# Kernel optimization log

Hardware: AMD Instinct MI355X
Metric: run time of the kernel (lower is better)

The kernel has to match this reference:

```python
import jax, jax.numpy as jnp
import numpy as np

EMB = 1024
NH = 16
HD = EMB // NH
FF = 4 * EMB
B, T = 2, 2048
LN_EPS = 1e-5


def setup_inputs() -> dict:
    key = jax.random.key(0)
    ks = jax.random.split(key, 16)
    s = 0.02
    return {
        "x": jax.random.normal(ks[0], (B, T, EMB), jnp.float32),
        "wq": jax.random.normal(ks[1], (EMB, EMB), jnp.float32) * s,
        "bq": jnp.zeros((EMB,), jnp.float32),
        "wk": jax.random.normal(ks[2], (EMB, EMB), jnp.float32) * s,
        "bk": jnp.zeros((EMB,), jnp.float32),
        "wv": jax.random.normal(ks[3], (EMB, EMB), jnp.float32) * s,
        "bv": jnp.zeros((EMB,), jnp.float32),
        "wo": jax.random.normal(ks[4], (EMB, EMB), jnp.float32) * s,
        "bo": jnp.zeros((EMB,), jnp.float32),
        "w1": jax.random.normal(ks[5], (EMB, FF), jnp.float32) * s,
        "b1": jnp.zeros((FF,), jnp.float32),
        "w2": jax.random.normal(ks[6], (FF, EMB), jnp.float32) * s,
        "b2": jnp.zeros((EMB,), jnp.float32),
        "ln1_g": jnp.ones((EMB,), jnp.float32),
        "ln1_b": jnp.zeros((EMB,), jnp.float32),
        "ln2_g": jnp.ones((EMB,), jnp.float32),
        "ln2_b": jnp.zeros((EMB,), jnp.float32),
        "alpha_attn": jnp.float32(0.5),
        "alpha_ff": jnp.float32(0.5),
    }


def _layernorm(x, g, b):
    mu = jnp.mean(x, axis=-1, keepdims=True)
    var = jnp.var(x, axis=-1, keepdims=True)
    return (x - mu) * jax.lax.rsqrt(var + LN_EPS) * g + b


def reference(x, wq, bq, wk, bk, wv, bv, wo, bo, w1, b1, w2, b2,
              ln1_g, ln1_b, ln2_g, ln2_b, alpha_attn, alpha_ff):
    residual = x
    x_ = _layernorm(x, ln1_g, ln1_b)
    # [B,T,E] -> [B,H,T,D]
    def heads(y):
        return y.reshape(B, T, NH, HD).transpose(0, 2, 1, 3)
    q = heads(x_ @ wq + bq)
    k = heads(x_ @ wk + bk)
    v = heads(x_ @ wv + bv)
    scores = jnp.einsum("bhqd,bhkd->bhqk", q, k) / np.sqrt(HD).astype(np.float32)
    causal = jnp.tril(jnp.ones((T, T), dtype=bool))
    scores = jnp.where(causal, scores, -jnp.inf)
    attn = jax.nn.softmax(scores, axis=-1)  # dropout is identity in eval mode
    out = jnp.einsum("bhqk,bhkd->bhqd", attn, v)
    out = out.transpose(0, 2, 1, 3).reshape(B, T, EMB)
    out = out @ wo + bo
    x = residual + alpha_attn * out
    x2 = _layernorm(x, ln2_g, ln2_b)
    ff = jax.nn.gelu(x2 @ w1 + b1, approximate=False) @ w2 + b2
    return x + alpha_ff * ff
```

## Files before the change

### kernel.cpp

```cpp
#include <hip/hip_runtime.h>
#include <cmath>

#define EMB 1024
#define NH 16
#define HD 64
#define FF_DIM 4096
#define BB 2
#define TT 2048
#define NTOK (BB * TT)
#define QKVS 3072
#define SC2F 0.18033688011112042f

typedef _Float16 f16x8 __attribute__((ext_vector_type(8)));
typedef _Float16 f16x4 __attribute__((ext_vector_type(4)));
typedef float f32x4 __attribute__((ext_vector_type(4)));

__device__ __forceinline__ float gelu_fast(float x) {
    float u = x * (1.f + 0.044715f * x * x);
    float e = exp2f(u * 2.302118751f);
    return x - x / (e + 1.f);
}

template <typename TIN>
__global__ __launch_bounds__(256) void ln_kernel(const TIN* __restrict__ xin,
                                                 _Float16* __restrict__ out,
                                                 const float* __restrict__ g,
                                                 const float* __restrict__ bv) {
    int tid = threadIdx.x;
    size_t base = (size_t)blockIdx.x * EMB;
    float v[4];
#pragma unroll
    for (int i = 0; i < 4; ++i) v[i] = (float)xin[base + i * 256 + tid];
    float s = v[0] + v[1] + v[2] + v[3];
    float ss = v[0] * v[0] + v[1] * v[1] + v[2] * v[2] + v[3] * v[3];
#pragma unroll
    for (int off = 32; off > 0; off >>= 1) {
        s += __shfl_down(s, off);
        ss += __shfl_down(ss, off);
    }
    __shared__ float red[8];
    int wave = tid >> 6;
    if ((tid & 63) == 0) { red[wave] = s; red[4 + wave] = ss; }
    __syncthreads();
    s = red[0] + red[1] + red[2] + red[3];
    ss = red[4] + red[5] + red[6] + red[7];
    float mu = s * (1.0f / EMB);
    float var = ss * (1.0f / EMB) - mu * mu;
    float rstd = rsqrtf(var + 1e-5f);
#pragma unroll
    for (int i = 0; i < 4; ++i) {
        int idx = i * 256 + tid;
        float y = (v[i] - mu) * rstd * g[idx] + bv[idx];
        out[base + idx] = (_Float16)y;
    }
}

__global__ __launch_bounds__(256) void prep0_kernel(const float* __restrict__ x,
                                                    _Float16* __restrict__ xn,
                                                    const float* __restrict__ ln1_g,
                                                    const float* __restrict__ ln1_b,
                                                    const float* __restrict__ wq,
                                                    const float* __restrict__ wk,
                                                    const float* __restrict__ wv,
                                                    const float* __restrict__ wo,
                                                    const float* __restrict__ bq,
                                                    const float* __restrict__ bk,
                                                    const float* __restrict__ bv,
                                                    _Float16* __restrict__ wqkvT,
                                                    _Float16* __restrict__ woT,
                                                    float* __restrict__ qkvbias) {
    __shared__ float tile[32][33];
    int blk = blockIdx.x;
    int tid = threadIdx.x;
    if (blk >= 4108) {
        size_t base = (size_t)(blk - 4108) * EMB;
        float v[4];
#pragma unroll
        for (int i = 0; i < 4; ++i) v[i] = x[base + i * 256 + tid];
        float s = v[0] + v[1] + v[2] + v[3];
        float ss = v[0] * v[0] + v[1] * v[1] + v[2] * v[2] + v[3] * v[3];
#pragma unroll
        for (int off = 32; off > 0; off >>= 1) {
            s += __shfl_down(s, off);
            ss += __shfl_down(ss, off);
        }
        float* red = &tile[0][0];
        int wave = tid >> 6;
        if ((tid & 63) == 0) { red[wave] = s; red[4 + wave] = ss; }
        __syncthreads();
        s = red[0] + red[1] + red[2] + red[3];
        ss = red[4] + red[5] + red[6] + red[7];
        float mu = s * (1.0f / EMB);
        float var = ss * (1.0f / EMB) - mu * mu;
        float rstd = rsqrtf(var + 1e-5f);
#pragma unroll
        for (int i = 0; i < 4; ++i) {
            int idx = i * 256 + tid;
            xn[base + idx] = (_Float16)((v[i] - mu) * rstd * ln1_g[idx] + ln1_b[idx]);
        }
        return;
    }
    if (blk >= 4096) {
        int i = (blk - 4096) * 256 + tid;
        qkvbias[i] = i < 1024 ? bq[i] : (i < 2048 ? bk[i - 1024] : bv[i - 2048]);
        return;
    }
    const float* W;
    _Float16* Wt;
    int t = blk & 1023;
    int z = blk >> 10;
    if (z == 0) { W = wq; Wt = wqkvT; }
    else if (z == 1) { W = wk; Wt = wqkvT + 1024 * 1024; }
    else if (z == 2) { W = wv; Wt = wqkvT + 2 * 1024 * 1024; }
    else { W = wo; Wt = woT; }
    int bx = (t & 31) * 32, by = (t >> 5) * 32;
    int tx = tid & 31, ty = tid >> 5;
#pragma unroll
    for (int i = 0; i < 32; i += 8)
        tile[ty + i][tx] = W[(size_t)(by + ty + i) * EMB + bx + tx];
    __syncthreads();
#pragma unroll
    for (int i = 0; i < 32; i += 8)
        Wt[(size_t)(bx + ty + i) * EMB + by + tx] = (_Float16)tile[tx][ty + i];
}

__global__ __launch_bounds__(256) void prep2_kernel(const float* __restrict__ w1,
                                                    const float* __restrict__ w2,
                                                    _Float16* __restrict__ w1T,
                                                    _Float16* __restrict__ w2T) {
    int b = blockIdx.x;
    const float* W;
    _Float16* Wt;
    int K, N, t;
    if (b < 4096) { W = w1; Wt = w1T; K = 1024; N = 4096; t = b; }
    else { W = w2; Wt = w2T; K = 4096; N = 1024; t = b - 4096; }
    int ntx = N >> 5;
    int bx = (t % ntx) * 32, by = (t / ntx) * 32;
    __shared__ float tile[32][33];
    int tx = threadIdx.x & 31, ty = threadIdx.x >> 5;
#pragma unroll
    for (int i = 0; i < 32; i += 8)
        tile[ty + i][tx] = W[(size_t)(by + ty + i) * N + bx + tx];
    __syncthreads();
#pragma unroll
    for (int i = 0; i < 32; i += 8)
        Wt[(size_t)(bx + ty + i) * K + by + tx] = (_Float16)tile[tx][ty + i];
}

__global__ __launch_bounds__(256) void vT_kernel(const _Float16* __restrict__ qkv,
                                                 _Float16* __restrict__ VtG) {
    __shared__ _Float16 tile[64][72];
    int tid = threadIdx.x;
    int bh = blockIdx.y;
    int b = bh >> 4, h = bh & 15;
    int t0 = blockIdx.x * 64;
    const _Float16* src = qkv + (size_t)b * TT * QKVS + 2048 + h * HD;
    int r = tid >> 3;
    int c8 = (tid & 7) * 8;
#pragma unroll
    for (int p = 0; p < 2; ++p)
        *(f16x8*)(&tile[r + p * 32][c8]) =
            *(const f16x8*)(src + (size_t)(t0 + r + p * 32) * QKVS + c8);
    __syncthreads();
#pragma unroll
    for (int p = 0; p < 2; ++p) {
        int d = r + p * 32;
        f16x8 v;
#pragma unroll
        for (int j = 0; j < 8; ++j) v[j] = tile[c8 + j][d];
        *(f16x8*)(VtG + ((size_t)bh * HD + d) * TT + t0 + c8) = v;
    }
}

template <int MODE>
__global__ __launch_bounds__(256) void gemm_f16t(const _Float16* __restrict__ A,
                                                 const _Float16* __restrict__ Bt,
                                                 const float* __restrict__ bias,
                                                 void* __restrict__ outp,
                                                 void* __restrict__ vtg,
                                                 int M, int N, int K, int lda, int ldb) {
    __shared__ _Float16 As[128][64];
    __shared__ _Float16 Bs[128][64];
    int tid = threadIdx.x;
    int lane = tid & 63, w = tid >> 6;
    int quad = lane >> 4, l15 = lane & 15;
    int wm = (w >> 1) * 64, wn = (w & 1) * 64;
    int bM = blockIdx.y * 128, bN = blockIdx.x * 128;
    int lr = lane >> 3;
    int lcs = ((lane & 7) ^ lr) * 8;
    int sw = l15 & 7;
    f32x4 acc[4][4] = {};

    const _Float16* Abase = A + (size_t)(bM + w * 32 + lr) * lda + lcs;
    const _Float16* Bbase = Bt + (size_t)(bN + w * 32 + lr) * ldb + lcs;

    for (int kt = 0; kt < K; kt += 64) {
#pragma unroll
        for (int i = 0; i < 4; ++i) {
            __builtin_amdgcn_global_load_lds(
                (const __attribute__((address_space(1))) void*)(Abase + (size_t)(i * 8) * lda + kt),
                (__attribute__((address_space(3))) void*)(&As[w * 32 + i * 8][0]), 16, 0, 0);
            __builtin_amdgcn_global_load_lds(
                (const __attribute__((address_space(1))) void*)(Bbase + (size_t)(i * 8) * ldb + kt),
                (__attribute__((address_space(3))) void*)(&Bs[w * 32 + i * 8][0]), 16, 0, 0);
        }
        __syncthreads();
#pragma unroll
        for (int ks = 0; ks < 2; ++ks) {
            f16x8 af[4], bf[4];
#pragma unroll
            for (int i = 0; i < 4; ++i) {
                int sc = ((ks * 4 + quad) ^ sw) * 8;
                af[i] = *(const f16x8*)(&As[wm + i * 16 + l15][sc]);
                bf[i] = *(const f16x8*)(&Bs[wn + i * 16 + l15][sc]);
            }
#pragma unroll
            for (int i = 0; i < 4; ++i)
#pragma unroll
                for (int j = 0; j < 4; ++j)
                    acc[i][j] = __builtin_amdgcn_mfma_f32_16x16x32_f16(af[i], bf[j], acc[i][j], 0, 0, 0);
        }
        __syncthreads();
    }

    if (MODE == 6 && vtg != nullptr && bN >= 2048) {
        int bb = bM >> 11;
        int tbase = (bM & 2047) + wm;
#pragma unroll
        for (int i = 0; i < 4; ++i)
#pragma unroll
            for (int j = 0; j < 4; ++j) {
                int hd = bN - 2048 + wn + j * 16;
                int col = 2048 + hd + l15;
                _Float16* dst = (_Float16*)vtg +
                    (((size_t)(bb * 16 + (hd >> 6)) * 64) + (hd & 63) + l15) * TT +
                    tbase + i * 16 + quad * 4;
                f16x4 ov;
#pragma unroll
                for (int r = 0; r < 4; ++r) ov[r] = (_Float16)(acc[i][j][r] + bias[col]);
                *(f16x4*)dst = ov;
            }
        return;
    }

#pragma unroll
    for (int i = 0; i < 4; ++i)
#pragma unroll
        for (int j = 0; j < 4; ++j)
#pragma unroll
            for (int r = 0; r < 4; ++r) {
                int row = bM + wm + i * 16 + quad * 4 + r;
                int col = bN + wn + j * 16 + l15;
                size_t idx = (size_t)row * N + col;
                float vv = acc[i][j][r] + bias[col];
                if (MODE == 6) {
                    if (bN < 1024) vv *= SC2F;
                    ((_Float16*)outp)[idx] = (_Float16)vv;
                } else {
                    ((_Float16*)outp)[idx] = (_Float16)gelu_fast(vv);
                }
            }
}

#define STAGE_PAIR(OB, TN, I)                                                            \
    {                                                                                    \
        size_t ko = (size_t)(TN) * 64;                                                   \
        __builtin_amdgcn_global_load_lds(                                                \
            (const __attribute__((address_space(1))) void*)(Ab + (size_t)((I) * 8) * lda + ko), \
            (__attribute__((address_space(3))) void*)(&As[OB][w * 32 + (I) * 8][0]), 16, 0, 0); \
        __builtin_amdgcn_global_load_lds(                                                \
            (const __attribute__((address_space(1))) void*)(Bb + (size_t)((I) * 8) * ldb + ko), \
            (__attribute__((address_space(3))) void*)(&Bs[OB][w * 32 + (I) * 8][0]), 16, 0, 0); \
    }
#define RD_A(CB, I, KS) (*(const f16x8*)(&As[CB][wr * 128 + (I) * 16 + l15][(((KS)*4 + quad) ^ sw) * 8]))
#define RD_B(CB, J, KS) (*(const f16x8*)(&Bs[CB][wc * 64 + (J) * 16 + l15][(((KS)*4 + quad) ^ sw) * 8]))
#define MMQ(I0, J0)                                                                      \
    _Pragma("unroll") for (int ks = 0; ks < 2; ++ks) {                                   \
        _Pragma("unroll") for (int ii = 0; ii < 4; ++ii) {                               \
            _Pragma("unroll") for (int jj = 0; jj < 2; ++jj)                             \
                acc[(I0) + ii][(J0) + jj] = __builtin_amdgcn_mfma_f32_16x16x32_f16(      \
                    af[ii][ks], bf[(J0) + jj][ks], acc[(I0) + ii][(J0) + jj], 0, 0, 0);  \
        }                                                                                \
    }

template <int MODE>
__global__ __launch_bounds__(512, 2) void gemm256(const _Float16* __restrict__ A,
                                                  const _Float16* __restrict__ Bt,
                                                  const float* __restrict__ bias,
                                                  void* __restrict__ outp,
                                                  void* __restrict__ vtg,
                                                  int M, int N, int K, int lda, int ldb) {
    __shared__ _Float16 As[2][256][64];
    __shared__ _Float16 Bs[2][256][64];
    int tid = threadIdx.x;
    int lane = tid & 63, w = tid >> 6;
    int quad = lane >> 4, l15 = lane & 15;
    int wr = w >> 2, wc = w & 3;
    int gx = gridDim.x;
    int nwg = gx * gridDim.y;
    int bid = blockIdx.y * gx + blockIdx.x;
    int cpx = nwg >> 3;
    int sbid = (bid & 7) * cpx + (bid >> 3);
    int bN = (sbid % gx) * 256;
    int bM = (sbid / gx) * 256;
    int lr = lane >> 3;
    int lcs = ((lane & 7) ^ lr) * 8;
    int sw = l15 & 7;
    f32x4 acc[8][4] = {};
    f16x8 af[4][2], bf[4][2];

    const _Float16* Ab = A + (size_t)(bM + w * 32 + lr) * lda + lcs;
    const _Float16* Bb = Bt + (size_t)(bN + w * 32 + lr) * ldb + lcs;
    const int NT = K >> 6;

#pragma unroll
    for (int i = 0; i < 4; ++i) STAGE_PAIR(0, 0, i);
    asm volatile("s_waitcnt vmcnt(0)" ::: "memory");
    __builtin_amdgcn_s_barrier();

    int cur = 0;
    for (int t = 0; t < NT; ++t) {
        int nxt = cur ^ 1;
        int tn = (t + 1 < NT) ? t + 1 : 0;
#pragma unroll
        for (int i = 0; i < 4; ++i) STAGE_PAIR(nxt, tn, i);
#pragma unroll
        for (int i = 0; i < 4; ++i) {
            af[i][0] = RD_A(cur, i, 0);
            af[i][1] = RD_A(cur, i, 1);
        }
        bf[0][0] = RD_B(cur, 0, 0); bf[0][1] = RD_B(cur, 0, 1);
        bf[1][0] = RD_B(cur, 1, 0); bf[1][1] = RD_B(cur, 1, 1);
        MMQ(0, 0);
        bf[2][0] = RD_B(cur, 2, 0); bf[2][1] = RD_B(cur, 2, 1);
        bf[3][0] = RD_B(cur, 3, 0); bf[3][1] = RD_B(cur, 3, 1);
        MMQ(0, 2);
#pragma unroll
        for (int i = 0; i < 4; ++i) {
            af[i][0] = RD_A(cur, 4 + i, 0);
            af[i][1] = RD_A(cur, 4 + i, 1);
        }
        MMQ(4, 0);
        MMQ(4, 2);
        asm volatile("s_waitcnt vmcnt(0)" ::: "memory");
        __builtin_amdgcn_s_barrier();
        cur = nxt;
    }

    if (MODE == 1 && vtg != nullptr && bN >= 2048) {
        int bb = bM >> 11;
#pragma unroll
        for (int i = 0; i < 8; ++i)
#pragma unroll
            for (int j = 0; j < 4; ++j) {
                int hd = bN - 2048 + wc * 64 + j * 16;
                int col = 2048 + hd + l15;
                int tb = (bM & 2047) + wr * 128 + i * 16 + quad * 4;
                _Float16* dst = (_Float16*)vtg +
                    (((size_t)(bb * 16 + (hd >> 6)) * 64) + (hd & 63) + l15) * TT + tb;
                f16x4 ov;
#pragma unroll
                for (int r = 0; r < 4; ++r) ov[r] = (_Float16)(acc[i][j][r] + bias[col]);
                *(f16x4*)dst = ov;
            }
        return;
    }

#pragma unroll
    for (int i = 0; i < 8; ++i)
#pragma unroll
        for (int j = 0; j < 4; ++j)
#pragma unroll
            for (int r = 0; r < 4; ++r) {
                int row = bM + wr * 128 + i * 16 + quad * 4 + r;
                int col = bN + wc * 64 + j * 16 + l15;
                size_t idx = (size_t)row * N + col;
                float vv = acc[i][j][r] + bias[col];
                if (MODE == 1) {
                    if (bN < 1024) vv *= SC2F;
                    ((_Float16*)outp)[idx] = (_Float16)vv;
                } else {
                    ((_Float16*)outp)[idx] = (_Float16)gelu_fast(vv);
                }
            }
}

template <int MODE>
__global__ __launch_bounds__(256) void gemm64(const _Float16* __restrict__ A,
                                              const _Float16* __restrict__ Bt,
                                              const float* __restrict__ bias,
                                              void* __restrict__ outp,
                                              const void* __restrict__ residp,
                                              const float* __restrict__ alphap,
                                              int M, int N, int K, int lda, int ldb) {
    __shared__ _Float16 As[128][64];
    __shared__ _Float16 Bs[64][64];
    int tid = threadIdx.x;
    int lane = tid & 63, w = tid >> 6;
    int quad = lane >> 4, l15 = lane & 15;
    int wm = w * 32;
    int bM = blockIdx.y * 128, bN = blockIdx.x * 64;
    int lr = lane >> 3;
    int lcs = ((lane & 7) ^ lr) * 8;
    int sw = l15 & 7;
    int kz = (MODE == 7) ? blockIdx.z * K : 0;
    f32x4 acc[2][4] = {};

    const _Float16* Abase = A + (size_t)(bM + w * 32 + lr) * lda + kz + lcs;
    const _Float16* Bbase = Bt + (size_t)(bN + w * 16 + lr) * ldb + kz + lcs;

    for (int kt = 0; kt < K; kt += 64) {
#pragma unroll
        for (int i = 0; i < 4; ++i)
            __builtin_amdgcn_global_load_lds(
                (const __attribute__((address_space(1))) void*)(Abase + (size_t)(i * 8) * lda + kt),
                (__attribute__((address_space(3))) void*)(&As[w * 32 + i * 8][0]), 16, 0, 0);
#pragma unroll
        for (int i = 0; i < 2; ++i)
            __builtin_amdgcn_global_load_lds(
                (const __attribute__((address_space(1))) void*)(Bbase + (size_t)(i * 8) * ldb + kt),
                (__attribute__((address_space(3))) void*)(&Bs[w * 16 + i * 8][0]), 16, 0, 0);
        __syncthreads();
#pragma unroll
        for (int ks = 0; ks < 2; ++ks) {
            int sc = ((ks * 4 + quad) ^ sw) * 8;
            f16x8 af[2], bf[4];
#pragma unroll
            for (int i = 0; i < 2; ++i)
                af[i] = *(const f16x8*)(&As[wm + i * 16 + l15][sc]);
#pragma unroll
            for (int j = 0; j < 4; ++j)
                bf[j] = *(const f16x8*)(&Bs[j * 16 + l15][sc]);
#pragma unroll
            for (int i = 0; i < 2; ++i)
#pragma unroll
                for (int j = 0; j < 4; ++j)
                    acc[i][j] = __builtin_amdgcn_mfma_f32_16x16x32_f16(af[i], bf[j], acc[i][j], 0, 0, 0);
        }
        __syncthreads();
    }

    float alpha = 0.f;
    if (MODE == 2 || MODE == 5) alpha = alphap[0];
    _Float16* pout = nullptr;
    if (MODE == 7) pout = blockIdx.z ? (_Float16*)(void*)residp : (_Float16*)outp;
#pragma unroll
    for (int i = 0; i < 2; ++i)
#pragma unroll
        for (int j = 0; j < 4; ++j)
#pragma unroll
            for (int r = 0; r < 4; ++r) {
                int row = bM + wm + i * 16 + quad * 4 + r;
                int col = bN + j * 16 + l15;
                size_t idx = (size_t)row * N + col;
                if (MODE == 7) {
                    pout[idx] = (_Float16)acc[i][j][r];
                } else if (MODE == 4) {
                    ((float*)outp)[idx] = acc[i][j][r];
                } else if (MODE == 2) {
                    float vv = acc[i][j][r] + bias[col];
                    float rsd = ((const float*)residp)[idx];
                    ((_Float16*)outp)[idx] = (_Float16)(rsd + alpha * vv);
                } else {
                    float vv = acc[i][j][r] + bias[col];
                    float prev = ((float*)outp)[idx];
                    float rsd = (float)((const _Float16*)residp)[idx];
                    ((float*)outp)[idx] = rsd + alpha * (prev + vv);
                }
            }
}

__global__ __launch_bounds__(256) void ff2_reduce_kernel(const _Float16* __restrict__ p0,
                                                         const _Float16* __restrict__ p1,
                                                         const _Float16* __restrict__ xmid,
                                                         const float* __restrict__ b2,
                                                         const float* __restrict__ alphap,
                                                         float* __restrict__ out) {
    int i = (blockIdx.x * 256 + threadIdx.x) * 8;
    float alpha = alphap[0];
    f16x8 a = *(const f16x8*)(p0 + i);
    f16x8 b = *(const f16x8*)(p1 + i);
    f16x8 xm = *(const f16x8*)(xmid + i);
    int col = i & 1023;
#pragma unroll
    for (int k = 0; k < 8; ++k)
        out[i + k] = (float)xm[k] + alpha * ((float)a[k] + (float)b[k] + b2[col + k]);
}

#define QT 64
#define NEG_BIG (-1e30f)
__global__ __launch_bounds__(512) void attn_mfma_kernel(const _Float16* __restrict__ qkv,
                                                        const _Float16* __restrict__ VtG,
                                                        _Float16* __restrict__ O) {
    __shared__ _Float16 Ks[64][72];
    __shared__ _Float16 Vt[64][72];
    __shared__ _Float16 Ps[8][16][68];
    int tid = threadIdx.x;
    int lane = tid & 63, w = tid >> 6;
    int quad = lane >> 4, l15 = lane & 15;
    int bh = blockIdx.x;
    int b = bh >> 4, h = bh & 15;
    int y = blockIdx.y;
    int seg = w >> 2, ws = w & 3;
    int qt = seg ? y : (31 - y);
    int q0 = qt * QT;
    int ntw = qt + 1;
    int ntmax = 32 - y;
    const _Float16* Qh = qkv + (size_t)b * TT * QKVS + h * HD;
    const _Float16* Kh = Qh + 1024;
    const _Float16* Vrows = VtG + (size_t)bh * HD * TT;

    int m0 = q0 + ws * 16;
    f16x8 aq0 = *(const f16x8*)(Qh + (size_t)(m0 + l15) * QKVS + quad * 8);
    f16x8 aq1 = *(const f16x8*)(Qh + (size_t)(m0 + l15) * QKVS + 32 + quad * 8);

    f32x4 Oacc[4] = {};
    float lrow[4] = {0.f, 0.f, 0.f, 0.f};

    int rr = tid >> 3;
    int c8 = (tid & 7) * 8;
    const _Float16* Kp = Kh + (size_t)rr * QKVS + c8;
    const _Float16* Vp = Vrows + (size_t)rr * TT + c8;

    f16x8 kreg = *(const f16x8*)(Kp);
    f16x8 vreg = *(const f16x8*)(Vp);

    for (int t = 0; t < ntmax; ++t) {
        int t0 = t * 64;
        __syncthreads();
        *(f16x8*)(&Ks[rr][c8]) = kreg;
        *(f16x8*)(&Vt[rr][c8]) = vreg;
        __syncthreads();
        if (t + 1 < ntmax) {
            kreg = *(const f16x8*)(Kp + (size_t)(t0 + 64) * QKVS);
            vreg = *(const f16x8*)(Vp + t0 + 64);
        }
        if (t >= ntw) continue;

        f32x4 Sacc[4] = {};
        __builtin_amdgcn_s_setprio(1);
#pragma unroll
        for (int nc = 0; nc < 4; ++nc) {
            f16x8 bk0 = *(const f16x8*)(&Ks[nc * 16 + l15][quad * 8]);
            f16x8 bk1 = *(const f16x8*)(&Ks[nc * 16 + l15][32 + quad * 8]);
            Sacc[nc] = __builtin_amdgcn_mfma_f32_16x16x32_f16(aq0, bk0, Sacc[nc], 0, 0, 0);
            Sacc[nc] = __builtin_amdgcn_mfma_f32_16x16x32_f16(aq1, bk1, Sacc[nc], 0, 0, 0);
        }
        __builtin_amdgcn_s_setprio(0);

        if (t0 == q0) {
#pragma unroll
            for (int nc = 0; nc < 4; ++nc) {
                int key = t0 + nc * 16 + l15;
#pragma unroll
                for (int i = 0; i < 4; ++i)
                    if (key > m0 + quad * 4 + i) Sacc[nc][i] = NEG_BIG;
            }
        }

#pragma unroll
        for (int nc = 0; nc < 4; ++nc)
#pragma unroll
            for (int i = 0; i < 4; ++i) {
                float p = exp2f(Sacc[nc][i]);
                lrow[i] += p;
                Ps[w][quad * 4 + i][nc * 16 + l15] = (_Float16)p;
            }
        __asm__ __volatile__("s_waitcnt lgkmcnt(0)" ::: "memory");

        f16x8 ap0 = *(const f16x8*)(&Ps[w][l15][quad * 8]);
        f16x8 ap1 = *(const f16x8*)(&Ps[w][l15][32 + quad * 8]);
        __builtin_amdgcn_s_setprio(1);
#pragma unroll
        for (int nc = 0; nc < 4; ++nc) {
            int d = nc * 16 + l15;
            f16x8 bv0 = *(const f16x8*)(&Vt[d][quad * 8]);
            f16x8 bv1 = *(const f16x8*)(&Vt[d][32 + quad * 8]);
            Oacc[nc] = __builtin_amdgcn_mfma_f32_16x16x32_f16(ap0, bv0, Oacc[nc], 0, 0, 0);
            Oacc[nc] = __builtin_amdgcn_mfma_f32_16x16x32_f16(ap1, bv1, Oacc[nc], 0, 0, 0);
        }
        __builtin_amdgcn_s_setprio(0);
    }

#pragma unroll
    for (int off = 1; off < 16; off <<= 1)
#pragma unroll
        for (int i = 0; i < 4; ++i) lrow[i] += __shfl_xor(lrow[i], off);
#pragma unroll
    for (int i = 0; i < 4; ++i) lrow[i] = 1.0f / lrow[i];
    _Float16* Oh = O + (size_t)b * TT * EMB + h * HD;
#pragma unroll
    for (int nc = 0; nc < 4; ++nc)
#pragma unroll
        for (int i = 0; i < 4; ++i) {
            int row = m0 + quad * 4 + i;
            Oh[(size_t)row * EMB + nc * 16 + l15] = (_Float16)(Oacc[nc][i] * lrow[i]);
        }
}

extern "C" void kernel_launch(void* const* d_in, const int* in_sizes, int n_in,
                              void* d_out, int out_size, void* d_ws, size_t ws_size,
                              hipStream_t stream) {
    const float* x = (const float*)d_in[0];
    const float* wq = (const float*)d_in[1];
    const float* bq = (const float*)d_in[2];
    const float* wk = (const float*)d_in[3];
    const float* bk = (const float*)d_in[4];
    const float* wv = (const float*)d_in[5];
    const float* bv = (const float*)d_in[6];
    const float* wo = (const float*)d_in[7];
    const float* bo = (const float*)d_in[8];
    const float* w1 = (const float*)d_in[9];
    const float* b1 = (const float*)d_in[10];
    const float* w2 = (const float*)d_in[11];
    const float* b2 = (const float*)d_in[12];
    const float* ln1_g = (const float*)d_in[13];
    const float* ln1_b = (const float*)d_in[14];
    const float* ln2_g = (const float*)d_in[15];
    const float* ln2_b = (const float*)d_in[16];
    const float* alpha_attn = (const float*)d_in[17];
    const float* alpha_ff = (const float*)d_in[18];

    const size_t SL = (size_t)8 * 1024 * 1024;
    char* ws = (char*)d_ws;
    _Float16* xn = (_Float16*)(ws);
    _Float16* qkv = (_Float16*)(ws + SL);
    _Float16* wqkvT = (_Float16*)(ws + 4 * SL);
    float* qkvbias = (float*)(ws + 4 * SL + 6 * 1024 * 1024);
    _Float16* attnout = (_Float16*)(ws);
    _Float16* xmid = (_Float16*)(ws + SL);
    _Float16* x2 = (_Float16*)(ws + 2 * SL);
    _Float16* w1T = (_Float16*)(ws);
    _Float16* w2T = (_Float16*)(ws + 3 * SL);
    _Float16* ff1 = (_Float16*)(ws + 4 * SL);
    bool bigws = ws_size >= (size_t)64 * 1024 * 1024;
    _Float16* VtG = bigws ? (_Float16*)(ws + 5 * SL) : (_Float16*)(ws + 4 * SL);
    _Float16* woT = bigws ? (_Float16*)(ws + 6 * SL) : (_Float16*)(ws + 5 * SL);
    _Float16* part0 = (_Float16*)(ws);
    _Float16* part1 = (_Float16*)(ws + 2 * SL);

    prep0_kernel<<<8204, 256, 0, stream>>>(x, xn, ln1_g, ln1_b, wq, wk, wv, wo,
                                           bq, bk, bv, wqkvT, woT, qkvbias);

    if (bigws) {
        gemm256<1><<<dim3(QKVS / 256, NTOK / 256), 512, 0, stream>>>(
            xn, wqkvT, qkvbias, qkv, (void*)VtG, NTOK, QKVS, EMB, EMB, EMB);
    } else {
        gemm_f16t<6><<<dim3(QKVS / 128, NTOK / 128), 256, 0, stream>>>(
            xn, wqkvT, qkvbias, qkv, nullptr, NTOK, QKVS, EMB, EMB, EMB);
        vT_kernel<<<dim3(TT / 64, BB * NH), 256, 0, stream>>>(qkv, VtG);
    }

    attn_mfma_kernel<<<dim3(BB * NH, TT / QT / 2), 512, 0, stream>>>(qkv, VtG, attnout);

    gemm64<2><<<dim3(EMB / 64, NTOK / 128), 256, 0, stream>>>(
        attnout, woT, bo, xmid, x, alpha_attn, NTOK, EMB, EMB, EMB, EMB);

    ln_kernel<_Float16><<<NTOK, 256, 0, stream>>>(xmid, x2, ln2_g, ln2_b);

    prep2_kernel<<<8192, 256, 0, stream>>>(w1, w2, w1T, w2T);

    if (bigws) {
        gemm256<0><<<dim3(FF_DIM / 256, NTOK / 256), 512, 0, stream>>>(
            x2, w1T, b1, ff1, nullptr, NTOK, FF_DIM, EMB, EMB, EMB);
        gemm64<7><<<dim3(EMB / 64, NTOK / 128, 2), 256, 0, stream>>>(
            ff1, w2T, nullptr, part0, part1, nullptr, NTOK, EMB, 2048, FF_DIM, FF_DIM);
        ff2_reduce_kernel<<<NTOK * EMB / 8 / 256, 256, 0, stream>>>(
            part0, part1, xmid, b2, alpha_ff, (float*)d_out);
    } else {
        const int NC = 2048;
        for (int hh = 0; hh < 2; ++hh) {
            const _Float16* w1Th = w1T + (size_t)hh * NC * EMB;
            const _Float16* w2Th = w2T + (size_t)hh * NC;
            gemm_f16t<1><<<dim3(NC / 128, NTOK / 128), 256, 0, stream>>>(
                x2, w1Th, b1 + hh * NC, ff1, nullptr, NTOK, NC, EMB, EMB, EMB);
            if (hh == 0)
                gemm64<4><<<dim3(EMB / 64, NTOK / 128), 256, 0, stream>>>(
                    ff1, w2Th, nullptr, d_out, nullptr, nullptr, NTOK, EMB, NC, NC, FF_DIM);
            else
                gemm64<5><<<dim3(EMB / 64, NTOK / 128), 256, 0, stream>>>(
                    ff1, w2Th, b2, d_out, xmid, alpha_ff, NTOK, EMB, NC, NC, FF_DIM);
        }
    }
}
```

Before: 358.2 us.

## Double-buffer LDS tiles in gemm64 to overlap global loads with MFMA

The gemm64 kernel now keeps two LDS buffers for the A and B tiles. It issues the direct global-to-LDS loads for the next K tile before computing on the current one, and replaces __syncthreads with an explicit vmcnt wait plus barrier. This is meant to hide global memory latency behind the MFMA work. It doubles LDS use per block, which may reduce occupancy, and the last iteration issues one redundant prefetch. An indentation change in the attention kernel is cosmetic.

```diff
diff --git a/kernel.cpp b/kernel.cpp
--- a/kernel.cpp
+++ b/kernel.cpp
@@ -393,8 +393,8 @@
                                               const void* __restrict__ residp,
                                               const float* __restrict__ alphap,
                                               int M, int N, int K, int lda, int ldb) {
-    __shared__ _Float16 As[128][64];
-    __shared__ _Float16 Bs[64][64];
+    __shared__ _Float16 As[2][128][64];
+    __shared__ _Float16 Bs[2][64][64];
     int tid = threadIdx.x;
     int lane = tid & 63, w = tid >> 6;
     int quad = lane >> 4, l15 = lane & 15;
@@ -409,35 +409,47 @@
     const _Float16* Abase = A + (size_t)(bM + w * 32 + lr) * lda + kz + lcs;
     const _Float16* Bbase = Bt + (size_t)(bN + w * 16 + lr) * ldb + kz + lcs;
 
-    for (int kt = 0; kt < K; kt += 64) {
-#pragma unroll
-        for (int i = 0; i < 4; ++i)
-            __builtin_amdgcn_global_load_lds(
-                (const __attribute__((address_space(1))) void*)(Abase + (size_t)(i * 8) * lda + kt),
-                (__attribute__((address_space(3))) void*)(&As[w * 32 + i * 8][0]), 16, 0, 0);
-#pragma unroll
-        for (int i = 0; i < 2; ++i)
-            __builtin_amdgcn_global_load_lds(
-                (const __attribute__((address_space(1))) void*)(Bbase + (size_t)(i * 8) * ldb + kt),
-                (__attribute__((address_space(3))) void*)(&Bs[w * 16 + i * 8][0]), 16, 0, 0);
-        __syncthreads();
+#define G64_STAGE(OB, KO)                                                                \
+    {                                                                                    \
+        _Pragma("unroll") for (int i = 0; i < 4; ++i)                                    \
+            __builtin_amdgcn_global_load_lds(                                            \
+                (const __attribute__((address_space(1))) void*)(Abase + (size_t)(i * 8) * lda + (KO)), \
+                (__attribute__((address_space(3))) void*)(&As[OB][w * 32 + i * 8][0]), 16, 0, 0); \
+        _Pragma("unroll") for (int i = 0; i < 2; ++i)                                    \
+            __builtin_amdgcn_global_load_lds(                                            \
+                (const __attribute__((address_space(1))) void*)(Bbase + (size_t)(i * 8) * ldb + (KO)), \
+                (__attribute__((address_space(3))) void*)(&Bs[OB][w * 16 + i * 8][0]), 16, 0, 0); \
+    }
+
+    G64_STAGE(0, 0);
+    asm volatile("s_waitcnt vmcnt(0)" ::: "memory");
+    __builtin_amdgcn_s_barrier();
+
+    const int NTt = K >> 6;
+    int cur = 0;
+    for (int t = 0; t < NTt; ++t) {
+        int nxt = cur ^ 1;
+        int ko = (t + 1 < NTt) ? (t + 1) * 64 : 0;
+        G64_STAGE(nxt, ko);
 #pragma unroll
         for (int ks = 0; ks < 2; ++ks) {
             int sc = ((ks * 4 + quad) ^ sw) * 8;
             f16x8 af[2], bf[4];
 #pragma unroll
             for (int i = 0; i < 2; ++i)
-                af[i] = *(const f16x8*)(&As[wm + i * 16 + l15][sc]);
+                af[i] = *(const f16x8*)(&As[cur][wm + i * 16 + l15][sc]);
 #pragma unroll
             for (int j = 0; j < 4; ++j)
-                bf[j] = *(const f16x8*)(&Bs[j * 16 + l15][sc]);
+                bf[j] = *(const f16x8*)(&Bs[cur][j * 16 + l15][sc]);
 #pragma unroll
             for (int i = 0; i < 2; ++i)
 #pragma unroll
                 for (int j = 0; j < 4; ++j)
                     acc[i][j] = __builtin_amdgcn_mfma_f32_16x16x32_f16(af[i], bf[j], acc[i][j], 0, 0, 0);
         }
-        __syncthreads();
+        asm volatile("s_waitcnt vmcnt(0)" ::: "memory");
+        __builtin_amdgcn_s_barrier();
+        cur = nxt;
     }
 
     float alpha = 0.f;
@@ -566,7 +578,7 @@
                 lrow[i] += p;
                 Ps[w][quad * 4 + i][nc * 16 + l15] = (_Float16)p;
             }
-        __asm__ __volatile__("s_waitcnt lgkmcnt(0)" ::: "memory");
+    __asm__ __volatile__("s_waitcnt lgkmcnt(0)" ::: "memory");
 
         f16x8 ap0 = *(const f16x8*)(&Ps[w][l15][quad * 8]);
         f16x8 ap1 = *(const f16x8*)(&Ps[w][l15][32 + quad * 8]);
```

New measurement: 358.3 us. Within noise of the previous version (+0.0%).

## Add double-buffered 256x128 split-K GEMM kernel for FF2 projection

Applied to the files above, without the earlier changes.

Replaces the 128x64 single-buffered split-K gemm64<7> for the second FFN matmul with a dedicated 512-thread kernel that uses 256x128 tiles, double-buffered LDS via global_load_lds with prefetch of the next K tile, and an XCD-aware block remapping. The aim is to raise arithmetic intensity per tile and overlap global-to-LDS loads with MFMA work. The grid shrinks to 8x16x2 = 256 blocks, which may lower occupancy, and each block uses about 96 KB of LDS. The dead MODE 7 path is removed from gemm64.

```diff
diff --git a/kernel.cpp b/kernel.cpp
--- a/kernel.cpp
+++ b/kernel.cpp
@@ -385,6 +385,94 @@
             }
 }
 
+__global__ __launch_bounds__(512) void gemm_ff2(const _Float16* __restrict__ A,
+                                                const _Float16* __restrict__ Bt,
+                                                _Float16* __restrict__ p0,
+                                                _Float16* __restrict__ p1,
+                                                int M, int N, int K, int lda, int ldb) {
+    __shared__ _Float16 As[2][256][64];
+    __shared__ _Float16 Bs[2][128][64];
+    int tid = threadIdx.x;
+    int lane = tid & 63, w = tid >> 6;
+    int quad = lane >> 4, l15 = lane & 15;
+    int wr = w >> 1, wc = w & 1;
+    int gx = gridDim.x;
+    int nwg = gx * gridDim.y;
+    int bid = blockIdx.y * gx + blockIdx.x;
+    int cpx = nwg >> 3;
+    int sbid = (bid & 7) * cpx + (bid >> 3);
+    int bN = (sbid % gx) * 128;
+    int bM = (sbid / gx) * 256;
+    int kz = blockIdx.z * K;
+    int lr = lane >> 3;
+    int lcs = ((lane & 7) ^ lr) * 8;
+    int sw = l15 & 7;
+    f32x4 acc[4][4] = {};
+    f16x8 af[4][2], bf[4][2];
+
+    const _Float16* Ab = A + (size_t)(bM + w * 32 + lr) * lda + kz + lcs;
+    const _Float16* Bb = Bt + (size_t)(bN + w * 16 + lr) * ldb + kz + lcs;
+    const int NT = K >> 6;
+
+#define FF2_STAGE(OB, TN)                                                                \
+    {                                                                                    \
+        size_t ko = (size_t)(TN) * 64;                                                   \
+        _Pragma("unroll") for (int i = 0; i < 4; ++i)                                    \
+            __builtin_amdgcn_global_load_lds(                                            \
+                (const __attribute__((address_space(1))) void*)(Ab + (size_t)(i * 8) * lda + ko), \
+                (__attribute__((address_space(3))) void*)(&As[OB][w * 32 + i * 8][0]), 16, 0, 0); \
+        _Pragma("unroll") for (int i = 0; i < 2; ++i)                                    \
+            __builtin_amdgcn_global_load_lds(                                            \
+                (const __attribute__((address_space(1))) void*)(Bb + (size_t)(i * 8) * ldb + ko), \
+                (__attribute__((address_space(3))) void*)(&Bs[OB][w * 16 + i * 8][0]), 16, 0, 0); \
+    }
+
+    FF2_STAGE(0, 0);
+    asm volatile("s_waitcnt vmcnt(0)" ::: "memory");
+    __builtin_amdgcn_s_barrier();
+
+    int cur = 0;
+    for (int t = 0; t < NT; ++t) {
+        int nxt = cur ^ 1;
+        int tn = (t + 1 < NT) ? t + 1 : 0;
+        FF2_STAGE(nxt, tn);
+#pragma unroll
+        for (int i = 0; i < 4; ++i) {
+#pragma unroll
+            for (int ks = 0; ks < 2; ++ks)
+                af[i][ks] = *(const f16x8*)(&As[cur][wr * 64 + i * 16 + l15][((ks * 4 + quad) ^ sw) * 8]);
+        }
+#pragma unroll
+        for (int j = 0; j < 4; ++j) {
+#pragma unroll
+            for (int ks = 0; ks < 2; ++ks)
+                bf[j][ks] = *(const f16x8*)(&Bs[cur][wc * 64 + j * 16 + l15][((ks * 4 + quad) ^ sw) * 8]);
+        }
+#pragma unroll
+        for (int ks = 0; ks < 2; ++ks)
+#pragma unroll
+            for (int i = 0; i < 4; ++i)
+#pragma unroll
+                for (int j = 0; j < 4; ++j)
+                    acc[i][j] = __builtin_amdgcn_mfma_f32_16x16x32_f16(af[i][ks], bf[j][ks], acc[i][j], 0, 0, 0);
+        asm volatile("s_waitcnt vmcnt(0)" ::: "memory");
+        __builtin_amdgcn_s_barrier();
+        cur = nxt;
+    }
+
+    _Float16* pout = blockIdx.z ? p1 : p0;
+#pragma unroll
+    for (int i = 0; i < 4; ++i)
+#pragma unroll
+        for (int j = 0; j < 4; ++j)
+#pragma unroll
+            for (int r = 0; r < 4; ++r) {
+                int row = bM + wr * 64 + i * 16 + quad * 4 + r;
+                int col = bN + wc * 64 + j * 16 + l15;
+                pout[(size_t)row * N + col] = (_Float16)acc[i][j][r];
+            }
+}
+
 template <int MODE>
 __global__ __launch_bounds__(256) void gemm64(const _Float16* __restrict__ A,
                                               const _Float16* __restrict__ Bt,
@@ -403,11 +491,10 @@
     int lr = lane >> 3;
     int lcs = ((lane & 7) ^ lr) * 8;
     int sw = l15 & 7;
-    int kz = (MODE == 7) ? blockIdx.z * K : 0;
     f32x4 acc[2][4] = {};
 
-    const _Float16* Abase = A + (size_t)(bM + w * 32 + lr) * lda + kz + lcs;
-    const _Float16* Bbase = Bt + (size_t)(bN + w * 16 + lr) * ldb + kz + lcs;
+    const _Float16* Abase = A + (size_t)(bM + w * 32 + lr) * lda + lcs;
+    const _Float16* Bbase = Bt + (size_t)(bN + w * 16 + lr) * ldb + lcs;
 
     for (int kt = 0; kt < K; kt += 64) {
 #pragma unroll
@@ -442,8 +529,6 @@
 
     float alpha = 0.f;
     if (MODE == 2 || MODE == 5) alpha = alphap[0];
-    _Float16* pout = nullptr;
-    if (MODE == 7) pout = blockIdx.z ? (_Float16*)(void*)residp : (_Float16*)outp;
 #pragma unroll
     for (int i = 0; i < 2; ++i)
 #pragma unroll
@@ -453,9 +538,7 @@
                 int row = bM + wm + i * 16 + quad * 4 + r;
                 int col = bN + j * 16 + l15;
                 size_t idx = (size_t)row * N + col;
-                if (MODE == 7) {
-                    pout[idx] = (_Float16)acc[i][j][r];
-                } else if (MODE == 4) {
+                if (MODE == 4) {
                     ((float*)outp)[idx] = acc[i][j][r];
                 } else if (MODE == 2) {
                     float vv = acc[i][j][r] + bias[col];
@@ -663,8 +746,8 @@
     if (bigws) {
         gemm256<0><<<dim3(FF_DIM / 256, NTOK / 256), 512, 0, stream>>>(
             x2, w1T, b1, ff1, nullptr, NTOK, FF_DIM, EMB, EMB, EMB);
-        gemm64<7><<<dim3(EMB / 64, NTOK / 128, 2), 256, 0, stream>>>(
-            ff1, w2T, nullptr, part0, part1, nullptr, NTOK, EMB, 2048, FF_DIM, FF_DIM);
+        gemm_ff2<<<dim3(EMB / 128, NTOK / 256, 2), 512, 0, stream>>>(
+            ff1, w2T, part0, part1, NTOK, EMB, 2048, FF_DIM, FF_DIM);
         ff2_reduce_kernel<<<NTOK * EMB / 8 / 256, 256, 0, stream>>>(
             part0, part1, xmid, b2, alpha_ff, (float*)d_out);
     } else {
```

Measured after the change: 343.9 us. 1.04x faster.
